# Kernel tuning notes

Hardware: AMD Instinct MI355X
Metric: run time of the kernel (lower is better)

## Reference

```python
import jax, jax.numpy as jnp
import numpy as np

B = 8192          # batch size
OBS = 128         # observation dim
HID = 512         # input_size / hidden_size
HEADS = 4         # num_input_heads
VSZ = 256         # input_value_size
NU = 64           # num_units (rim_num)
K = 8             # top-k
NOPT = 16         # option_num


def setup_inputs() -> dict:
    key = jax.random.key(0)
    ks = jax.random.split(key, 8)
    return {
        "x": jax.random.normal(ks[0], (B, OBS), dtype=jnp.float32),
        "option": jax.random.randint(ks[1], (B,), 0, NOPT),
        "pre_fc_w": jax.random.normal(ks[2], (OBS, HID), dtype=jnp.float32) * (OBS ** -0.5),
        "pre_fc_b": jax.random.normal(ks[3], (HID,), dtype=jnp.float32) * 0.01,
        "value_w": jax.random.normal(ks[4], (HID, HEADS * VSZ), dtype=jnp.float32) * (HID ** -0.5),
        "value_b": jax.random.normal(ks[5], (HEADS * VSZ,), dtype=jnp.float32) * 0.01,
        "p_w": jax.random.normal(ks[6], (NOPT, NU), dtype=jnp.float32),
        "p_b": jax.random.normal(ks[7], (NU,), dtype=jnp.float32),
    }


def reference(x, option, pre_fc_w, pre_fc_b, value_w, value_b, p_w, p_b):
    b = x.shape[0]
    # pre_fc: [B, OBS] -> [B, HID]
    h = x @ pre_fc_w + pre_fc_b
    # concat null input slot -> [B, 2, HID]
    h2 = jnp.stack([h, jnp.zeros_like(h)], axis=1)
    # one-hot option + null slot -> [B, 2, NOPT]
    oh = jax.nn.one_hot(option, NOPT, dtype=jnp.float32)
    oh2 = jnp.stack([oh, jnp.zeros_like(oh)], axis=1)
    # value projection, split heads, mean over heads -> [B, 2, VSZ]
    v = (h2 @ value_w + value_b).reshape(b, 2, HEADS, VSZ)
    value_layer = jnp.mean(v, axis=2)
    # attention scores: einsum('bio,on->bni') -> [B, NU, 2]
    scores = jnp.einsum('bio,on->bni', oh2, p_w)
    # bias: p_b for real slot, zeros for null slot
    pb = jnp.stack([jnp.broadcast_to(p_b, (b, NU)), jnp.zeros((b, NU), jnp.float32)], axis=2)
    scores = scores + pb
    # top-k unit mask over not-null scores [B, NU]
    not_null = scores[:, :, 0]
    _, topk_idx = jax.lax.top_k(not_null, K)  # [B, K]
    mask = jnp.zeros((b, NU), jnp.float32).at[jnp.arange(b)[:, None], topk_idx].set(1.0)
    # softmax over the 2 slots (dropout is identity at eval)
    probs = jax.nn.softmax(scores, axis=-1)  # [B, NU, 2]
    # attention readout, masked, mean over units -> [B, VSZ]
    inputs = jnp.einsum('bns,bsv->bnv', probs, value_layer) * mask[:, :, None]
    return jnp.mean(inputs, axis=1)
```

## Files before the change

kernel.cpp:

```cpp
#include <hip/hip_runtime.h>
#include <hip/hip_bf16.h>

#define B_N   8192
#define OBS   128
#define HID   512
#define VSZ   256
#define NU    64
#define TOPK  8
#define NOPT  16
#define KEXT  160

typedef __bf16 bf16_t;
typedef __bf16 bf16x8 __attribute__((ext_vector_type(8)));
typedef float  f32x4  __attribute__((ext_vector_type(4)));

#define OFF_A    0u
#define OFF_DP   256u
#define OFF_MT   2048u

__launch_bounds__(1024)
__global__ void k_wmt(const float* __restrict__ vw, const float* __restrict__ pw,
                      const float* __restrict__ pb, const float* __restrict__ p_w,
                      const float* __restrict__ p_b, const float* __restrict__ vb,
                      bf16_t* __restrict__ mt, float* __restrict__ A,
                      float* __restrict__ Dp) {
    const int tid = threadIdx.x;

    if (blockIdx.x == 32) {
        int wvi = tid >> 6;
        if (wvi < 4) {
            int lane = tid & 63;
            #pragma unroll
            for (int oo = 0; oo < 4; ++oo) {
                int o = wvi * 4 + oo;
                float cur = p_w[o * NU + lane] + p_b[lane];
                float sum = 0.f;
                #pragma unroll
                for (int t = 0; t < TOPK; ++t) {
                    float m = cur;
                    #pragma unroll
                    for (int off = 32; off >= 1; off >>= 1)
                        m = fmaxf(m, __shfl_xor(m, off));
                    sum += 1.f / (1.f + expf(-m));
                    unsigned long long bal = __ballot(cur == m);
                    int first = __ffsll(bal) - 1;
                    if (lane == first) cur = -1e30f;
                }
                if (lane == 0) A[o] = sum * (1.f / NU);
            }
        }
        if (tid >= 256 && tid < 512) {
            int v = tid & 255;
            Dp[v] = 0.03125f * ((vb[v] + vb[v + VSZ]) + (vb[v + 2 * VSZ] + vb[v + 3 * VSZ]));
        }
        return;
    }

    __shared__ float wl[HID][8];
    __shared__ float cpart[16][8];

    const int v0 = blockIdx.x * 8;

    #pragma unroll
    for (int r = 0; r < 4; ++r) {
        int e  = tid + r * 1024;
        int j  = e >> 3, vi = e & 7;
        const float* p = vw + j * (4 * VSZ) + v0 + vi;
        wl[j][vi] = 0.25f * ((p[0] + p[VSZ]) + (p[2 * VSZ] + p[3 * VSZ]));
    }
    __syncthreads();

    {
        int k  = tid >> 3, vi = tid & 7;
        const float* pr = pw + k * HID;
        float a0 = 0.f, a1 = 0.f, a2 = 0.f, a3 = 0.f;
        #pragma unroll 4
        for (int j = 0; j < HID; j += 4) {
            f32x4 p = *(const f32x4*)(pr + j);
            a0 += p[0] * wl[j + 0][vi];
            a1 += p[1] * wl[j + 1][vi];
            a2 += p[2] * wl[j + 2][vi];
            a3 += p[3] * wl[j + 3][vi];
        }
        mt[(v0 + vi) * KEXT + k] = (bf16_t)((a0 + a1) + (a2 + a3));
    }

    if (tid < 128) {
        int jq = tid >> 3, cvi = tid & 7;
        const float* pbq = pb + jq * 32;
        float s = 0.f;
        #pragma unroll 4
        for (int j = 0; j < 32; ++j) s += pbq[j] * wl[jq * 32 + j][cvi];
        cpart[jq][cvi] = s;
    }
    __syncthreads();
    if (tid < 8) {
        float s = 0.f;
        #pragma unroll
        for (int q = 0; q < 16; ++q) s += cpart[q][tid];
        mt[(v0 + tid) * KEXT + 128] = (bf16_t)s;
    }
    if (tid < 256) {
        int pvi = tid >> 5, kk = tid & 31;
        if (kk < 31) mt[(v0 + pvi) * KEXT + 129 + kk] = (bf16_t)0.f;
    }
}

__launch_bounds__(256)
__global__ void k_main(const float* __restrict__ x, const bf16_t* __restrict__ mt,
                       const int* __restrict__ opt, const float* __restrict__ A,
                       const float* __restrict__ Dp, float* __restrict__ out) {
    const int wave = threadIdx.x >> 6;
    const int lane = threadIdx.x & 63;
    const int mrow = lane & 15;
    const int quad = lane >> 4;
    const int r0   = blockIdx.x * 64 + wave * 16;
    const int c0   = blockIdx.y * 128;

    bf16x8 af[5];
    {
        const float* xr = x + (r0 + mrow) * OBS + quad * 8;
        f32x4 lo[4], hi[4];
        #pragma unroll
        for (int kt = 0; kt < 4; ++kt) {
            lo[kt] = *(const f32x4*)(xr + kt * 32);
            hi[kt] = *(const f32x4*)(xr + kt * 32 + 4);
        }
        #pragma unroll
        for (int kt = 0; kt < 4; ++kt) {
            bf16x8 a;
            a[0] = (bf16_t)lo[kt][0]; a[1] = (bf16_t)lo[kt][1];
            a[2] = (bf16_t)lo[kt][2]; a[3] = (bf16_t)lo[kt][3];
            a[4] = (bf16_t)hi[kt][0]; a[5] = (bf16_t)hi[kt][1];
            a[6] = (bf16_t)hi[kt][2]; a[7] = (bf16_t)hi[kt][3];
            af[kt] = a;
        }
        bf16x8 a;
        #pragma unroll
        for (int j = 0; j < 8; ++j) a[j] = (bf16_t)0.f;
        if (quad == 0) a[0] = (bf16_t)1.0f;
        af[4] = a;
    }

    float av[4];
    #pragma unroll
    for (int r = 0; r < 4; ++r)
        av[r] = A[opt[r0 + quad * 4 + r]];

    f32x4 acc[8];
    #pragma unroll
    for (int t = 0; t < 8; ++t) acc[t] = (f32x4){0.f, 0.f, 0.f, 0.f};

    const bf16_t* mb = mt + (c0 + mrow) * KEXT + quad * 8;
    #pragma unroll
    for (int kt = 0; kt < 5; ++kt) {
        #pragma unroll
        for (int t = 0; t < 8; ++t) {
            bf16x8 b = *(const bf16x8*)(mb + t * 16 * KEXT + kt * 32);
            acc[t] = __builtin_amdgcn_mfma_f32_16x16x32_bf16(af[kt], b, acc[t], 0, 0, 0);
        }
    }

    #pragma unroll
    for (int r = 0; r < 4; ++r) {
        int row = r0 + quad * 4 + r;
        float* orow = out + row * VSZ;
        #pragma unroll
        for (int t = 0; t < 8; ++t) {
            int col = c0 + t * 16 + mrow;
            orow[col] = av[r] * acc[t][r] + Dp[col];
        }
    }
}

extern "C" void kernel_launch(void* const* d_in, const int* in_sizes, int n_in,
                              void* d_out, int out_size, void* d_ws, size_t ws_size,
                              hipStream_t stream) {
    const float* x        = (const float*)d_in[0];
    const int*   option   = (const int*)  d_in[1];
    const float* pre_fc_w = (const float*)d_in[2];
    const float* pre_fc_b = (const float*)d_in[3];
    const float* value_w  = (const float*)d_in[4];
    const float* value_b  = (const float*)d_in[5];
    const float* p_w      = (const float*)d_in[6];
    const float* p_b      = (const float*)d_in[7];
    float* out = (float*)d_out;

    char* ws = (char*)d_ws;
    float*  A    = (float*) (ws + OFF_A);
    float*  Dp   = (float*) (ws + OFF_DP);
    bf16_t* mt   = (bf16_t*)(ws + OFF_MT);

    k_wmt <<<dim3(33), dim3(1024), 0, stream>>>(value_w, pre_fc_w, pre_fc_b,
                                                p_w, p_b, value_b, mt, A, Dp);
    k_main<<<dim3(B_N / 64, VSZ / 128), dim3(256), 0, stream>>>(x, mt, option, A, Dp, out);
}
```

Measured before the change: 94.82 us.

## Compute folded weight matrix with MFMA in weight-prep kernel

The weight-prep kernel now computes the folded pre_fc×value_w product (and the bias row) with bf16 MFMA instructions instead of scalar FP32 dot products. Each block handles 16 value columns with 256 threads, down from 8 columns with 1024 threads, so the launch shrinks to 17 blocks. The head-averaged weights are staged in shared memory as bf16. This targets the serial FMA latency of the prep kernel, at the cost of extra bf16 rounding on an intermediate and fewer threads per block.

```diff
diff --git a/kernel.cpp b/kernel.cpp
--- a/kernel.cpp
+++ b/kernel.cpp
@@ -18,7 +18,7 @@
 #define OFF_DP   256u
 #define OFF_MT   2048u
 
-__launch_bounds__(1024)
+__launch_bounds__(256)
 __global__ void k_wmt(const float* __restrict__ vw, const float* __restrict__ pw,
                       const float* __restrict__ pb, const float* __restrict__ p_w,
                       const float* __restrict__ p_b, const float* __restrict__ vb,
@@ -26,83 +26,85 @@
                       float* __restrict__ Dp) {
     const int tid = threadIdx.x;
 
-    if (blockIdx.x == 32) {
-        int wvi = tid >> 6;
-        if (wvi < 4) {
-            int lane = tid & 63;
+    if (blockIdx.x == 16) {
+        int lane = tid & 63;
+        int wvi  = tid >> 6;
+        #pragma unroll
+        for (int oo = 0; oo < 4; ++oo) {
+            int o = wvi * 4 + oo;
+            float cur = p_w[o * NU + lane] + p_b[lane];
+            float sum = 0.f;
             #pragma unroll
-            for (int oo = 0; oo < 4; ++oo) {
-                int o = wvi * 4 + oo;
-                float cur = p_w[o * NU + lane] + p_b[lane];
-                float sum = 0.f;
+            for (int t = 0; t < TOPK; ++t) {
+                float m = cur;
                 #pragma unroll
-                for (int t = 0; t < TOPK; ++t) {
-                    float m = cur;
-                    #pragma unroll
-                    for (int off = 32; off >= 1; off >>= 1)
-                        m = fmaxf(m, __shfl_xor(m, off));
-                    sum += 1.f / (1.f + expf(-m));
-                    unsigned long long bal = __ballot(cur == m);
-                    int first = __ffsll(bal) - 1;
-                    if (lane == first) cur = -1e30f;
-                }
-                if (lane == 0) A[o] = sum * (1.f / NU);
+                for (int off = 32; off >= 1; off >>= 1)
+                    m = fmaxf(m, __shfl_xor(m, off));
+                sum += 1.f / (1.f + expf(-m));
+                unsigned long long bal = __ballot(cur == m);
+                int first = __ffsll(bal) - 1;
+                if (lane == first) cur = -1e30f;
             }
+            if (lane == 0) A[o] = sum * (1.f / NU);
         }
-        if (tid >= 256 && tid < 512) {
-            int v = tid & 255;
-            Dp[v] = 0.03125f * ((vb[v] + vb[v + VSZ]) + (vb[v + 2 * VSZ] + vb[v + 3 * VSZ]));
-        }
+        Dp[tid] = 0.03125f * ((vb[tid] + vb[tid + VSZ]) + (vb[tid + 2 * VSZ] + vb[tid + 3 * VSZ]));
         return;
     }
 
-    __shared__ float wl[HID][8];
-    __shared__ float cpart[16][8];
+    const int v0 = blockIdx.x * 16;
+    __shared__ bf16_t wt[16][520];
 
-    const int v0 = blockIdx.x * 8;
-
-    #pragma unroll
-    for (int r = 0; r < 4; ++r) {
-        int e  = tid + r * 1024;
-        int j  = e >> 3, vi = e & 7;
-        const float* p = vw + j * (4 * VSZ) + v0 + vi;
-        wl[j][vi] = 0.25f * ((p[0] + p[VSZ]) + (p[2 * VSZ] + p[3 * VSZ]));
+    {
+        const int vi = tid & 15;
+        const int jb = tid >> 4;
+        #pragma unroll 8
+        for (int p = 0; p < 32; ++p) {
+            int j = p * 16 + jb;
+            const float* src = vw + j * (4 * VSZ) + v0 + vi;
+            float s = 0.25f * ((src[0] + src[VSZ]) + (src[2 * VSZ] + src[3 * VSZ]));
+            wt[vi][j] = (bf16_t)s;
+        }
     }
     __syncthreads();
 
-    {
-        int k  = tid >> 3, vi = tid & 7;
-        const float* pr = pw + k * HID;
-        float a0 = 0.f, a1 = 0.f, a2 = 0.f, a3 = 0.f;
-        #pragma unroll 4
-        for (int j = 0; j < HID; j += 4) {
-            f32x4 p = *(const f32x4*)(pr + j);
-            a0 += p[0] * wl[j + 0][vi];
-            a1 += p[1] * wl[j + 1][vi];
-            a2 += p[2] * wl[j + 2][vi];
-            a3 += p[3] * wl[j + 3][vi];
+    const int lane = tid & 63;
+    const int w    = tid >> 6;
+    const int mrow = lane & 15;
+    const int quad = lane >> 4;
+    const bf16_t* wrow = &wt[mrow][quad * 8];
+
+    for (int t = w; t < 10; t += 4) {
+        int  k0   = t * 16;
+        bool bias = (t == 8);
+        bool act  = bias ? (mrow == 0) : true;
+        const float* brow = bias ? (pb + quad * 8)
+                                 : (pw + (k0 + mrow) * HID + quad * 8);
+        f32x4 acc = {0.f, 0.f, 0.f, 0.f};
+        #pragma unroll
+        for (int kt = 0; kt < 16; ++kt) {
+            bf16x8 a = *(const bf16x8*)(wrow + kt * 32);
+            bf16x8 b;
+            if (act) {
+                f32x4 lo = *(const f32x4*)(brow + kt * 32);
+                f32x4 hi = *(const f32x4*)(brow + kt * 32 + 4);
+                b[0] = (bf16_t)lo[0]; b[1] = (bf16_t)lo[1];
+                b[2] = (bf16_t)lo[2]; b[3] = (bf16_t)lo[3];
+                b[4] = (bf16_t)hi[0]; b[5] = (bf16_t)hi[1];
+                b[6] = (bf16_t)hi[2]; b[7] = (bf16_t)hi[3];
+            } else {
+                #pragma unroll
+                for (int jj = 0; jj < 8; ++jj) b[jj] = (bf16_t)0.f;
+            }
+            acc = __builtin_amdgcn_mfma_f32_16x16x32_bf16(a, b, acc, 0, 0, 0);
         }
-        mt[(v0 + vi) * KEXT + k] = (bf16_t)((a0 + a1) + (a2 + a3));
+        #pragma unroll
+        for (int r = 0; r < 4; ++r)
+            mt[(v0 + quad * 4 + r) * KEXT + k0 + mrow] = (bf16_t)acc[r];
     }
 
-    if (tid < 128) {
-        int jq = tid >> 3, cvi = tid & 7;
-        const float* pbq = pb + jq * 32;
-        float s = 0.f;
-        #pragma unroll 4
-        for (int j = 0; j < 32; ++j) s += pbq[j] * wl[jq * 32 + j][cvi];
-        cpart[jq][cvi] = s;
-    }
-    __syncthreads();
-    if (tid < 8) {
-        float s = 0.f;
-        #pragma unroll
-        for (int q = 0; q < 16; ++q) s += cpart[q][tid];
-        mt[(v0 + tid) * KEXT + 128] = (bf16_t)s;
-    }
-    if (tid < 256) {
-        int pvi = tid >> 5, kk = tid & 31;
-        if (kk < 31) mt[(v0 + pvi) * KEXT + 129 + kk] = (bf16_t)0.f;
+    {
+        int vv = tid >> 4, kk = tid & 15;
+        mt[(v0 + vv) * KEXT + 144 + kk] = (bf16_t)0.f;
     }
 }
 
@@ -191,7 +193,7 @@
     float*  Dp   = (float*) (ws + OFF_DP);
     bf16_t* mt   = (bf16_t*)(ws + OFF_MT);
 
-    k_wmt <<<dim3(33), dim3(1024), 0, stream>>>(value_w, pre_fc_w, pre_fc_b,
-                                                p_w, p_b, value_b, mt, A, Dp);
+    k_wmt <<<dim3(17), dim3(256), 0, stream>>>(value_w, pre_fc_w, pre_fc_b,
+                                               p_w, p_b, value_b, mt, A, Dp);
     k_main<<<dim3(B_N / 64, VSZ / 128), dim3(256), 0, stream>>>(x, mt, option, A, Dp, out);
 }
```

After: 95.97 us. No clear change (+1.2%).
